# Optimization experiments

Measured on AMD Instinct MI355X. Metric: run time of the kernel, lower is better.

The kernel has to match this reference:

```python
import jax, jax.numpy as jnp
import numpy as np

B, N, C, NT = 32, 512, 32, 24   # batch, frames, channels-per-token, tokens
H, DH = 8, 48                   # heads, dim_head (DH % NT == 0 -> CS = 2)
E = H * DH                      # encode_dim = 384
IN = C * NT                     # in_dim = 768
OUT = 768                       # out_dim


def setup_inputs() -> dict:
    key = jax.random.key(0)
    ks = jax.random.split(key, 12)
    s = lambda fan_in: 1.0 / np.sqrt(fan_in)
    return {
        "x": jax.random.normal(ks[0], (B, N, C, NT), dtype=jnp.float32),
        "Wqkv_t": jax.random.uniform(ks[1], (IN, 3 * E), jnp.float32, -s(IN), s(IN)),
        "bqkv_t": jax.random.uniform(ks[2], (3 * E,), jnp.float32, -s(IN), s(IN)),
        "Wqkv_s": jax.random.uniform(ks[3], (IN, 3 * E), jnp.float32, -s(IN), s(IN)),
        "bqkv_s": jax.random.uniform(ks[4], (3 * E,), jnp.float32, -s(IN), s(IN)),
        "Wts": jax.random.uniform(ks[5], (2 * E, 2 * E), jnp.float32, -s(2 * E), s(2 * E)),
        "bts": jax.random.uniform(ks[6], (2 * E,), jnp.float32, -s(2 * E), s(2 * E)),
        "Wfc_t": jax.random.uniform(ks[7], (E, OUT), jnp.float32, -s(E), s(E)),
        "bfc_t": jax.random.uniform(ks[8], (OUT,), jnp.float32, -s(E), s(E)),
        "Wfc_s": jax.random.uniform(ks[9], (E, OUT), jnp.float32, -s(E), s(E)),
        "bfc_s": jax.random.uniform(ks[10], (OUT,), jnp.float32, -s(E), s(E)),
    }


def reference(x, Wqkv_t, bqkv_t, Wqkv_s, bqkv_s, Wts, bts, Wfc_t, bfc_t, Wfc_s, bfc_s):
    b, n, c, nt = x.shape
    cs = DH // nt  # channels per token inside a head (=2)
    xf = x.reshape(b, n, c * nt)                       # (b, n, in_dim)

    # --- temporal attention over the n (frame) axis ---
    qkv_t = (xf @ Wqkv_t + bqkv_t).reshape(b, n, 3, H, DH)
    qkv_t = jnp.transpose(qkv_t, (2, 0, 3, 1, 4))      # (3, b, H, n, DH)
    qt, kt, vt = qkv_t[0], qkv_t[1], qkv_t[2]
    attn_t = jax.nn.softmax(
        jnp.einsum('bhnd,bhmd->bhnm', qt, kt) / jnp.sqrt(jnp.float32(DH)), axis=-1)
    x_t = jnp.einsum('bhnm,bhmd->bnhd', attn_t, vt).reshape(b, n, E)

    # --- spatial attention over the nt (token) axis (note: unscaled, per source) ---
    qkv_s = (xf @ Wqkv_s + bqkv_s).reshape(b, n, 3, H, DH)
    qkv_s = jnp.transpose(qkv_s, (2, 0, 1, 3, 4)).reshape(3, b * n, H, cs, nt)
    qs, ks_, vs = qkv_s[0], qkv_s[1], qkv_s[2]         # (b*n, H, cs, nt)
    attn_s = jax.nn.softmax(jnp.einsum('ghct,ghcu->ghtu', qs, ks_), axis=-1)
    x_s = jnp.einsum('ghtu,ghcu->ghct', attn_s, vs)     # (b*n, H, cs, nt)
    x_s = x_s.reshape(b * n, H, cs * nt).reshape(b, n, E)

    # --- learned gating fusion ---
    alpha = jnp.concatenate([x_t, x_s], axis=-1).mean(axis=1, keepdims=True)  # (b,1,2E)
    alpha = (alpha @ Wts + bts).reshape(b, 1, E, 2)
    alpha = jax.nn.softmax(alpha, axis=-1)
    y = (x_t * alpha[:, :, :, 0]) @ Wfc_t + bfc_t + (x_s * alpha[:, :, :, 1]) @ Wfc_s + bfc_s
    return y  # dropout is identity in inference
```

## Files before the change

### kernel.cpp

```cpp
#include <hip/hip_runtime.h>
#include <hip/hip_bf16.h>


typedef __attribute__((ext_vector_type(8))) short s16x8;
typedef __attribute__((ext_vector_type(4))) float f32x4;

__device__ __forceinline__ float lo2f(uint u) { return __uint_as_float(u << 16); }
__device__ __forceinline__ float hi2f(uint u) { return __uint_as_float(u & 0xffff0000u); }
__device__ __forceinline__ ushort f2bu(float f) {
    union { __hip_bfloat16 h; ushort u; } c; c.h = __float2bfloat16(f); return c.u;
}
__device__ __forceinline__ uint pk2(float a, float b) {
    return (uint)f2bu(a) | ((uint)f2bu(b) << 16);
}
__device__ __forceinline__ void gload16(const void* g, void* l) {
    __builtin_amdgcn_global_load_lds((const __attribute__((address_space(1))) void*)g,
                                     (__attribute__((address_space(3))) void*)l, 16, 0, 0);
}

__device__ __forceinline__ void transpose_blk(
    const float* __restrict__ W, ushort* __restrict__ Bt,
    int task, int KT, int N, int Kt, int koff, int noff, float (*t)[33])
{
    const int k0 = (task % KT) * 32;
    const int n0 = (task / KT) * 32;
    const int r = threadIdx.x >> 3, cq = threadIdx.x & 7;
    float4 v = *(const float4*)(W + (size_t)(k0 + r) * N + n0 + cq * 4);
    t[r][cq * 4 + 0] = v.x; t[r][cq * 4 + 1] = v.y;
    t[r][cq * 4 + 2] = v.z; t[r][cq * 4 + 3] = v.w;
    __syncthreads();
    ushort4 o;
    o.x = f2bu(t[cq * 4 + 0][r]); o.y = f2bu(t[cq * 4 + 1][r]);
    o.z = f2bu(t[cq * 4 + 2][r]); o.w = f2bu(t[cq * 4 + 3][r]);
    *(ushort4*)(Bt + (size_t)(noff + n0 + r) * Kt + koff + k0 + cq * 4) = o;
}

__global__ __launch_bounds__(256) void prep(
    const float* __restrict__ x, ushort* __restrict__ xb,
    const float* __restrict__ bqkv_t, const float* __restrict__ bqkv_s,
    float* __restrict__ bias2,
    const float* __restrict__ Wqkv_t, const float* __restrict__ Wqkv_s,
    ushort* __restrict__ wbuf,
    const float* __restrict__ Wfc_t, const float* __restrict__ Wfc_s,
    ushort* __restrict__ wbuf2)
{
    __shared__ float t[32][33];
    const int bid = blockIdx.x;
    if (bid < 6144) {
        const int i = bid * 256 + threadIdx.x;
        const float4* p = (const float4*)x + (size_t)i * 2;
        float4 a = p[0], b = p[1];
        uint4 o;
        o.x = pk2(a.x, a.y); o.y = pk2(a.z, a.w);
        o.z = pk2(b.x, b.y); o.w = pk2(b.z, b.w);
        ((uint4*)xb)[i] = o;
    } else if (bid < 6153) {
        const int i = (bid - 6144) * 256 + threadIdx.x;
        bias2[i] = (i < 1152) ? bqkv_t[i] : bqkv_s[i - 1152];
    } else if (bid < 7017) {
        transpose_blk(Wqkv_t, wbuf, bid - 6153, 24, 1152, 768, 0, 0, t);
    } else if (bid < 7881) {
        transpose_blk(Wqkv_s, wbuf, bid - 7017, 24, 1152, 768, 0, 1152, t);
    } else if (bid < 8169) {
        transpose_blk(Wfc_t, wbuf2, bid - 7881, 12, 768, 768, 0, 0, t);
    } else {
        transpose_blk(Wfc_s, wbuf2, bid - 8169, 12, 768, 768, 384, 0, t);
    }
}

template<int OUTBF16, int NBIAS>
__global__ __launch_bounds__(256, 2) void gemm128p(
    const ushort* __restrict__ A, const ushort* __restrict__ Bt,
    const float* __restrict__ bias0, const float* __restrict__ bias1,
    void* __restrict__ Cout, int M, int N, int K)
{
    __shared__ ushort smem[32768];
    const int tid = threadIdx.x;
    const int m0 = blockIdx.x * 128;
    const int n0 = blockIdx.y * 128;
    const int lane = tid & 63;
    const int wr = tid >> 7;
    const int wc = (tid >> 6) & 1;
    const int lr = lane & 15;
    const int g = lane >> 4;

    f32x4 acc[4][4];
#pragma unroll
    for (int i = 0; i < 4; ++i)
#pragma unroll
        for (int j = 0; j < 4; ++j) acc[i][j] = (f32x4){0.f, 0.f, 0.f, 0.f};

    int rowT[4], kqs[4];
#pragma unroll
    for (int i = 0; i < 4; ++i) {
        const int task = tid + 256 * i;
        rowT[i] = task >> 3;
        kqs[i] = (task & 7) ^ (rowT[i] & 7);
    }

    auto stage = [&](int buf, int k0) {
        ushort* dA = &smem[buf * 16384];
        ushort* dB = &smem[buf * 16384 + 8192];
#pragma unroll
        for (int i = 0; i < 4; ++i) {
            gload16(A + (size_t)(m0 + rowT[i]) * K + k0 + (kqs[i] << 3),
                    dA + (tid + 256 * i) * 8);
            gload16(Bt + (size_t)(n0 + rowT[i]) * K + k0 + (kqs[i] << 3),
                    dB + (tid + 256 * i) * 8);
        }
    };

    stage(0, 0);
    const int nt = K >> 6;
    for (int t = 0; t < nt; ++t) {
        const int cur = t & 1;
        if (t + 1 < nt) {
            stage(cur ^ 1, (t + 1) << 6);
            asm volatile("s_waitcnt vmcnt(8)" ::: "memory");
        } else {
            asm volatile("s_waitcnt vmcnt(0)" ::: "memory");
        }
        __builtin_amdgcn_sched_barrier(0);
        __builtin_amdgcn_s_barrier();
        __builtin_amdgcn_sched_barrier(0);

        const ushort* As = &smem[cur * 16384];
        const ushort* Bs = &smem[cur * 16384 + 8192];
#pragma unroll
        for (int half = 0; half < 2; ++half) {
            s16x8 af[4], bfv[4];
#pragma unroll
            for (int i = 0; i < 4; ++i) {
                const int row = wr * 64 + 16 * i + lr;
                af[i] = *(const s16x8*)&As[row * 64
                         + (((4 * half + g) ^ (row & 7)) << 3)];
            }
#pragma unroll
            for (int j = 0; j < 4; ++j) {
                const int row = wc * 64 + 16 * j + lr;
                bfv[j] = *(const s16x8*)&Bs[row * 64
                          + (((4 * half + g) ^ (row & 7)) << 3)];
            }
#pragma unroll
            for (int i = 0; i < 4; ++i)
#pragma unroll
                for (int j = 0; j < 4; ++j)
                    acc[i][j] = __builtin_amdgcn_mfma_f32_16x16x32_bf16(
                        af[i], bfv[j], acc[i][j], 0, 0, 0);
        }
        __builtin_amdgcn_sched_barrier(0);
        __builtin_amdgcn_s_barrier();
    }

    const int c0 = n0 + wc * 64 + lr;
    float bsum[4];
#pragma unroll
    for (int j = 0; j < 4; ++j) {
        bsum[j] = bias0[c0 + 16 * j];
        if (NBIAS == 2) bsum[j] += bias1[c0 + 16 * j];
    }
    const int r0 = m0 + wr * 64 + g * 4;
#pragma unroll
    for (int i = 0; i < 4; ++i) {
        const int row = r0 + 16 * i;
#pragma unroll
        for (int j = 0; j < 4; ++j) {
            const int col = c0 + 16 * j;
#pragma unroll
            for (int v = 0; v < 4; ++v) {
                const float val = acc[i][j][v] + bsum[j];
                if (OUTBF16)
                    ((ushort*)Cout)[(size_t)(row + v) * N + col] = f2bu(val);
                else
                    ((float*)Cout)[(size_t)(row + v) * N + col] = val;
            }
        }
    }
}

__global__ __launch_bounds__(256, 4) void attn_temporal(
    const ushort* __restrict__ qkv, ushort* __restrict__ xcat)
{
    const int wg = blockIdx.x;
    const int cx = wg & 7, rx = wg >> 3;
    const int id = ((rx >> 2) << 5) + 4 * cx + (rx & 3);
    const int qt = id & 3;
    const int h = (id >> 2) & 7;
    const int b = id >> 5;

    const int tid = threadIdx.x;
    const int w = tid >> 6;
    const int lane = tid & 63;
    const int lr = lane & 15;
    const int g = lane >> 4;

    __shared__ ushort Ks[64 * 64];
    __shared__ ushort Vt[48 * 64];
    __shared__ ushort Pl[4][32 * 72];
    uint* KsU = (uint*)Ks;
    uint* VtU = (uint*)Vt;

    ((uint4*)Ks)[tid] = make_uint4(0u, 0u, 0u, 0u);
    ((uint4*)Ks)[256 + tid] = make_uint4(0u, 0u, 0u, 0u);
    __syncthreads();

    const uint* qkvu = (const uint*)qkv;
    const int qrow0 = qt * 128 + w * 32;

    s16x8 qf[2][2];
#pragma unroll
    for (int n = 0; n < 2; ++n) {
        const size_t rb = (size_t)(b * 512 + qrow0 + 16 * n + lr) * 2304 + h * 48 + 8 * g;
        qf[n][0] = *(const s16x8*)(qkv + rb);
        qf[n][1] = (g < 2) ? *(const s16x8*)(qkv + rb + 32)
                           : (s16x8){0, 0, 0, 0, 0, 0, 0, 0};
    }

    int p_[3], du_[3];
#pragma unroll
    for (int i = 0; i < 3; ++i) {
        const int idx = tid + 256 * i;
        p_[i] = idx / 24;
        du_[i] = idx % 24;
    }
    uint rk[3][2], rv[3][2];

    auto stage_load = [&](int kv0) {
#pragma unroll
        for (int i = 0; i < 3; ++i) {
            const uint* s0 = qkvu + (size_t)(b * 512 + kv0 + 2 * p_[i]) * 1152
                                  + 192 + h * 24 + du_[i];
            rk[i][0] = s0[0];    rk[i][1] = s0[1152];
            rv[i][0] = s0[192];  rv[i][1] = s0[192 + 1152];
        }
    };
    auto stage_write = [&]() {
#pragma unroll
        for (int i = 0; i < 3; ++i) {
            const int p = p_[i], du = du_[i];
            KsU[(2 * p) * 32 + ((((du >> 2) ^ ((2 * p) & 7)) << 2) | (du & 3))] = rk[i][0];
            KsU[(2 * p + 1) * 32 + ((((du >> 2) ^ ((2 * p + 1) & 7)) << 2) | (du & 3))] = rk[i][1];
            const uint w0 = (rv[i][0] & 0xffffu) | (rv[i][1] << 16);
            const uint w1 = (rv[i][0] >> 16) | (rv[i][1] & 0xffff0000u);
            const int vb = (((p >> 2) ^ (du & 7)) << 2) | (p & 3);
            VtU[(2 * du) * 32 + vb] = w0;
            VtU[(2 * du + 1) * 32 + vb] = w1;
        }
    };

    f32x4 o[2][3];
#pragma unroll
    for (int mq = 0; mq < 2; ++mq)
#pragma unroll
        for (int nd = 0; nd < 3; ++nd) o[mq][nd] = (f32x4){0.f, 0.f, 0.f, 0.f};
    float mrun[2] = {-3.0e38f, -3.0e38f};
    float lsum[2] = {0.f, 0.f};
    float corrv[2];
    const float scale = 0.14433756729740643f;

    stage_load(0);
    stage_write();
    __syncthreads();

    for (int t = 0; t < 8; ++t) {
        if (t < 7) stage_load((t + 1) * 64);

        f32x4 sa[4][2];
#pragma unroll
        for (int m = 0; m < 4; ++m)
#pragma unroll
            for (int n = 0; n < 2; ++n) sa[m][n] = (f32x4){0.f, 0.f, 0.f, 0.f};
        __builtin_amdgcn_s_setprio(1);
#pragma unroll
        for (int ks = 0; ks < 2; ++ks)
#pragma unroll
            for (int m = 0; m < 4; ++m) {
                s16x8 kf = *(const s16x8*)&Ks[(16 * m + lr) * 64
                                              + (((g + 4 * ks) ^ (lr & 7)) << 3)];
#pragma unroll
                for (int n = 0; n < 2; ++n)
                    sa[m][n] = __builtin_amdgcn_mfma_f32_16x16x32_bf16(
                        kf, qf[n][ks], sa[m][n], 0, 0, 0);
            }
        __builtin_amdgcn_s_setprio(0);

#pragma unroll
        for (int n = 0; n < 2; ++n) {
            float tmax = -3.0e38f;
#pragma unroll
            for (int m = 0; m < 4; ++m)
#pragma unroll
                for (int v = 0; v < 4; ++v) tmax = fmaxf(tmax, sa[m][n][v]);
            tmax = fmaxf(tmax, __shfl_xor(tmax, 16));
            tmax = fmaxf(tmax, __shfl_xor(tmax, 32));
            float mnew = fmaxf(mrun[n], tmax * scale);
            float corr = __expf(mrun[n] - mnew);
            mrun[n] = mnew;
            float psum = 0.f;
#pragma unroll
            for (int m = 0; m < 4; ++m) {
                float p0 = __expf(fmaf(sa[m][n][0], scale, -mnew));
                float p1 = __expf(fmaf(sa[m][n][1], scale, -mnew));
                float p2 = __expf(fmaf(sa[m][n][2], scale, -mnew));
                float p3 = __expf(fmaf(sa[m][n][3], scale, -mnew));
                psum += (p0 + p1) + (p2 + p3);
                const int base = (16 * n + lr) * 72 + 16 * m + 4 * g;
                *(uint*)&Pl[w][base] = pk2(p0, p1);
                *(uint*)&Pl[w][base + 2] = pk2(p2, p3);
            }
            psum += __shfl_xor(psum, 16);
            psum += __shfl_xor(psum, 32);
            lsum[n] = lsum[n] * corr + psum;
            corrv[n] = corr;
        }

#pragma unroll
        for (int mq = 0; mq < 2; ++mq)
#pragma unroll
            for (int nd = 0; nd < 3; ++nd)
#pragma unroll
                for (int v = 0; v < 4; ++v) o[mq][nd][v] *= corrv[mq];

        __builtin_amdgcn_s_setprio(1);
#pragma unroll
        for (int ks = 0; ks < 2; ++ks) {
            s16x8 vf[3];
#pragma unroll
            for (int nd = 0; nd < 3; ++nd)
                vf[nd] = *(const s16x8*)&Vt[(16 * nd + lr) * 64
                                            + (((g + 4 * ks) ^ (lr >> 1)) << 3)];
#pragma unroll
            for (int mq = 0; mq < 2; ++mq) {
                s16x8 pf = *(const s16x8*)&Pl[w][(16 * mq + lr) * 72 + 8 * g + 32 * ks];
#pragma unroll
                for (int nd = 0; nd < 3; ++nd)
                    o[mq][nd] = __builtin_amdgcn_mfma_f32_16x16x32_bf16(
                        vf[nd], pf, o[mq][nd], 0, 0, 0);
            }
        }
        __builtin_amdgcn_s_setprio(0);
        __syncthreads();
        if (t < 7) stage_write();
        __syncthreads();
    }

#pragma unroll
    for (int mq = 0; mq < 2; ++mq) {
        const float li = 1.f / lsum[mq];
        const int qrow = qrow0 + 16 * mq + lr;
        ushort* dst = xcat + (size_t)(b * 512 + qrow) * 768 + h * 48;
#pragma unroll
        for (int nd = 0; nd < 3; ++nd) {
            uint2 o2;
            o2.x = pk2(o[mq][nd][0] * li, o[mq][nd][1] * li);
            o2.y = pk2(o[mq][nd][2] * li, o[mq][nd][3] * li);
            *(uint2*)(dst + 16 * nd + 4 * g) = o2;
        }
    }
}

__global__ __launch_bounds__(192) void attn_spatial(
    const ushort* __restrict__ qkv, ushort* __restrict__ xcat)
{
    const int g = blockIdx.x;
    __shared__ float row[1152];
    const uint* qkvu = (const uint*)qkv;
#pragma unroll
    for (int i = 0; i < 3; ++i) {
        int idx = threadIdx.x + 192 * i;
        uint u = qkvu[(size_t)g * 1152 + 576 + idx];
        row[2 * idx] = lo2f(u); row[2 * idx + 1] = hi2f(u);
    }
    __syncthreads();

    const int h = threadIdx.x / 24;
    const int t = threadIdx.x % 24;
    const float* q = &row[h * 48];
    const float* k = &row[384 + h * 48];
    const float* v = &row[768 + h * 48];
    const float q0 = q[t], q1 = q[24 + t];

    float s[24];
    float mx = -3.0e38f;
#pragma unroll
    for (int u = 0; u < 24; ++u) {
        s[u] = q0 * k[u] + q1 * k[24 + u];
        mx = fmaxf(mx, s[u]);
    }
    float l = 0.f;
#pragma unroll
    for (int u = 0; u < 24; ++u) { s[u] = __expf(s[u] - mx); l += s[u]; }
    const float inv = 1.f / l;
    float o0 = 0.f, o1 = 0.f;
#pragma unroll
    for (int u = 0; u < 24; ++u) {
        o0 = fmaf(s[u], v[u], o0);
        o1 = fmaf(s[u], v[24 + u], o1);
    }
    ushort* dst = xcat + (size_t)g * 768 + 384 + h * 48;
    dst[t] = f2bu(o0 * inv);
    dst[24 + t] = f2bu(o1 * inv);
}

__global__ __launch_bounds__(256) void colsum(
    const ushort* __restrict__ xcat, float* __restrict__ partial)
{
    const int b = blockIdx.x, ch = blockIdx.y, part = blockIdx.z;
    const int e = ch * 256 + threadIdx.x;
    const int n0 = part * 64;
    float s = 0.f;
    for (int n = 0; n < 64; ++n)
        s += __uint_as_float((uint)xcat[((size_t)(b * 512 + n0 + n)) * 768 + e] << 16);
    partial[((size_t)(b * 8 + part)) * 768 + e] = s;
}

__global__ __launch_bounds__(256) void alpha_gate(
    const float* __restrict__ partial, const float* __restrict__ Wts,
    const float* __restrict__ bts, float* __restrict__ gate)
{
    const int b = blockIdx.x;
    const int j0 = blockIdx.y * 128;
    __shared__ float av[768];
    __shared__ float psum[2][128];

    for (int i = threadIdx.x; i < 768; i += 256) {
        float s = 0.f;
#pragma unroll
        for (int p = 0; p < 8; ++p)
            s += partial[((size_t)(b * 8 + p)) * 768 + i];
        av[i] = s * (1.0f / 512.0f);
    }
    __syncthreads();

    const int jl = threadIdx.x & 127;
    const int seg = threadIdx.x >> 7;
    const int j = j0 + jl;
    const float* Wp = Wts + (size_t)(seg * 384) * 768 + j;
    const float* avp = av + seg * 384;
    float a0 = 0.f, a1 = 0.f, a2 = 0.f, a3 = 0.f;
    float a4 = 0.f, a5 = 0.f, a6 = 0.f, a7 = 0.f;
#pragma unroll 4
    for (int k = 0; k < 384; k += 8) {
        a0 = fmaf(avp[k + 0], Wp[(size_t)(k + 0) * 768], a0);
        a1 = fmaf(avp[k + 1], Wp[(size_t)(k + 1) * 768], a1);
        a2 = fmaf(avp[k + 2], Wp[(size_t)(k + 2) * 768], a2);
        a3 = fmaf(avp[k + 3], Wp[(size_t)(k + 3) * 768], a3);
        a4 = fmaf(avp[k + 4], Wp[(size_t)(k + 4) * 768], a4);
        a5 = fmaf(avp[k + 5], Wp[(size_t)(k + 5) * 768], a5);
        a6 = fmaf(avp[k + 6], Wp[(size_t)(k + 6) * 768], a6);
        a7 = fmaf(avp[k + 7], Wp[(size_t)(k + 7) * 768], a7);
    }
    psum[seg][jl] = ((a0 + a1) + (a2 + a3)) + ((a4 + a5) + (a6 + a7));
    __syncthreads();

    if (threadIdx.x < 128)
        av[threadIdx.x] = psum[0][threadIdx.x] + psum[1][threadIdx.x]
                        + bts[j0 + threadIdx.x];
    __syncthreads();
    if (threadIdx.x < 64) {
        const int e = (j0 >> 1) + threadIdx.x;
        float x0 = av[2 * threadIdx.x], x1 = av[2 * threadIdx.x + 1];
        float m = fmaxf(x0, x1);
        float e0 = __expf(x0 - m), e1 = __expf(x1 - m);
        float inv = 1.f / (e0 + e1);
        gate[(size_t)b * 768 + e] = e0 * inv;
        gate[(size_t)b * 768 + 384 + e] = e1 * inv;
    }
}

__global__ __launch_bounds__(256) void gate_mul(
    const ushort* __restrict__ xcat, const float* __restrict__ gate,
    ushort* __restrict__ xg)
{
    const int i = blockIdx.x * 256 + threadIdx.x;
    const int m = i / 96;
    const int k = (i % 96) * 8;
    const int b = m >> 9;
    uint4 u = ((const uint4*)xcat)[i];
    const float* g = gate + (size_t)b * 768 + k;
    float4 g0 = *(const float4*)g;
    float4 g1 = *(const float4*)(g + 4);
    uint4 o;
    o.x = pk2(lo2f(u.x) * g0.x, hi2f(u.x) * g0.y);
    o.y = pk2(lo2f(u.y) * g0.z, hi2f(u.y) * g0.w);
    o.z = pk2(lo2f(u.z) * g1.x, hi2f(u.z) * g1.y);
    o.w = pk2(lo2f(u.w) * g1.z, hi2f(u.w) * g1.w);
    ((uint4*)xg)[i] = o;
}

extern "C" void kernel_launch(void* const* d_in, const int* in_sizes, int n_in,
                              void* d_out, int out_size, void* d_ws, size_t ws_size,
                              hipStream_t stream)
{
    const float* x      = (const float*)d_in[0];
    const float* Wqkv_t = (const float*)d_in[1];
    const float* bqkv_t = (const float*)d_in[2];
    const float* Wqkv_s = (const float*)d_in[3];
    const float* bqkv_s = (const float*)d_in[4];
    const float* Wts    = (const float*)d_in[5];
    const float* bts    = (const float*)d_in[6];
    const float* Wfc_t  = (const float*)d_in[7];
    const float* bfc_t  = (const float*)d_in[8];
    const float* Wfc_s  = (const float*)d_in[9];
    const float* bfc_s  = (const float*)d_in[10];
    float* out = (float*)d_out;

    char* w = (char*)d_ws;
    ushort* qkv2   = (ushort*)(w);
    ushort* xg     = qkv2;
    ushort* xcat   = (ushort*)(w + 75497472);
    ushort* xb     = (ushort*)(w + 100663296);
    ushort* wbuf   = (ushort*)(w + 125829120);
    ushort* wbuf2  = (ushort*)(w + 129368064);
    float*  partial= (float*)(w + 130547712);
    float*  gate   = (float*)(w + 131334144);
    float*  bias2  = (float*)(w + 131432448);

    const dim3 blk256(256);

    prep<<<dim3(8457), blk256, 0, stream>>>(
        x, xb, bqkv_t, bqkv_s, bias2, Wqkv_t, Wqkv_s, wbuf, Wfc_t, Wfc_s, wbuf2);

    gemm128p<1, 1><<<dim3(128, 18), blk256, 0, stream>>>(
        xb, wbuf, bias2, nullptr, qkv2, 16384, 2304, 768);

    attn_temporal<<<dim3(1024), blk256, 0, stream>>>(qkv2, xcat);
    attn_spatial<<<dim3(16384), dim3(192), 0, stream>>>(qkv2, xcat);

    colsum<<<dim3(32, 3, 8), blk256, 0, stream>>>(xcat, partial);
    alpha_gate<<<dim3(32, 6), blk256, 0, stream>>>(partial, Wts, bts, gate);
    gate_mul<<<dim3(6144), blk256, 0, stream>>>(xcat, gate, xg);

    gemm128p<0, 2><<<dim3(128, 6), blk256, 0, stream>>>(
        xg, wbuf2, bfc_t, bfc_s, out, 16384, 768, 768);
}
```

Before: 190.4 us.

## Merge spatial attention into temporal attention launch and skip small rescales

```diff
diff --git a/kernel.cpp b/kernel.cpp
--- a/kernel.cpp
+++ b/kernel.cpp
@@ -178,9 +178,58 @@
     }
 }
 
-__global__ __launch_bounds__(256, 4) void attn_temporal(
+__global__ __launch_bounds__(256, 4) void attn_fused(
     const ushort* __restrict__ qkv, ushort* __restrict__ xcat)
 {
+    __shared__ ushort Ks[64 * 64];
+    __shared__ ushort Vt[48 * 64];
+    __shared__ ushort Pl[4][32 * 72];
+    const int tid = threadIdx.x;
+    const uint* qkvu = (const uint*)qkv;
+
+    if (blockIdx.x >= 1024) {
+        const int g = blockIdx.x - 1024;
+        float* row = (float*)Ks;
+        if (tid < 192) {
+#pragma unroll
+            for (int i = 0; i < 3; ++i) {
+                int idx = tid + 192 * i;
+                uint u = qkvu[(size_t)g * 1152 + 576 + idx];
+                row[2 * idx] = lo2f(u); row[2 * idx + 1] = hi2f(u);
+            }
+        }
+        __syncthreads();
+        if (tid < 192) {
+            const int h = tid / 24;
+            const int t = tid % 24;
+            const float* q = &row[h * 48];
+            const float* k = &row[384 + h * 48];
+            const float* v = &row[768 + h * 48];
+            const float q0 = q[t], q1 = q[24 + t];
+            float s[24];
+            float mx = -3.0e38f;
+#pragma unroll
+            for (int u = 0; u < 24; ++u) {
+                s[u] = q0 * k[u] + q1 * k[24 + u];
+                mx = fmaxf(mx, s[u]);
+            }
+            float l = 0.f;
+#pragma unroll
+            for (int u = 0; u < 24; ++u) { s[u] = __expf(s[u] - mx); l += s[u]; }
+            const float inv = 1.f / l;
+            float o0 = 0.f, o1 = 0.f;
+#pragma unroll
+            for (int u = 0; u < 24; ++u) {
+                o0 = fmaf(s[u], v[u], o0);
+                o1 = fmaf(s[u], v[24 + u], o1);
+            }
+            ushort* dst = xcat + (size_t)g * 768 + 384 + h * 48;
+            dst[t] = f2bu(o0 * inv);
+            dst[24 + t] = f2bu(o1 * inv);
+        }
+        return;
+    }
+
     const int wg = blockIdx.x;
     const int cx = wg & 7, rx = wg >> 3;
     const int id = ((rx >> 2) << 5) + 4 * cx + (rx & 3);
@@ -188,15 +237,10 @@
     const int h = (id >> 2) & 7;
     const int b = id >> 5;
 
-    const int tid = threadIdx.x;
     const int w = tid >> 6;
     const int lane = tid & 63;
     const int lr = lane & 15;
     const int g = lane >> 4;
-
-    __shared__ ushort Ks[64 * 64];
-    __shared__ ushort Vt[48 * 64];
-    __shared__ ushort Pl[4][32 * 72];
     uint* KsU = (uint*)Ks;
     uint* VtU = (uint*)Vt;
 
@@ -204,7 +248,6 @@
     ((uint4*)Ks)[256 + tid] = make_uint4(0u, 0u, 0u, 0u);
     __syncthreads();
 
-    const uint* qkvu = (const uint*)qkv;
     const int qrow0 = qt * 128 + w * 32;
 
     s16x8 qf[2][2];
@@ -284,6 +327,7 @@
             }
         __builtin_amdgcn_s_setprio(0);
 
+        bool nogrow[2];
 #pragma unroll
         for (int n = 0; n < 2; ++n) {
             float tmax = -3.0e38f;
@@ -293,8 +337,10 @@
                 for (int v = 0; v < 4; ++v) tmax = fmaxf(tmax, sa[m][n][v]);
             tmax = fmaxf(tmax, __shfl_xor(tmax, 16));
             tmax = fmaxf(tmax, __shfl_xor(tmax, 32));
-            float mnew = fmaxf(mrun[n], tmax * scale);
-            float corr = __expf(mrun[n] - mnew);
+            const float tmax_s = tmax * scale;
+            nogrow[n] = __all(tmax_s <= mrun[n] + 4.f);
+            float mnew = nogrow[n] ? mrun[n] : fmaxf(mrun[n], tmax_s);
+            float corr = nogrow[n] ? 1.f : __expf(mrun[n] - mnew);
             mrun[n] = mnew;
             float psum = 0.f;
 #pragma unroll
@@ -314,12 +360,14 @@
             corrv[n] = corr;
         }
 
-#pragma unroll
-        for (int mq = 0; mq < 2; ++mq)
-#pragma unroll
-            for (int nd = 0; nd < 3; ++nd)
-#pragma unroll
-                for (int v = 0; v < 4; ++v) o[mq][nd][v] *= corrv[mq];
+        if (!(nogrow[0] && nogrow[1])) {
+#pragma unroll
+            for (int mq = 0; mq < 2; ++mq)
+#pragma unroll
+                for (int nd = 0; nd < 3; ++nd)
+#pragma unroll
+                    for (int v = 0; v < 4; ++v) o[mq][nd][v] *= corrv[mq];
+        }
 
         __builtin_amdgcn_s_setprio(1);
 #pragma unroll
@@ -357,49 +405,6 @@
             *(uint2*)(dst + 16 * nd + 4 * g) = o2;
         }
     }
-}
-
-__global__ __launch_bounds__(192) void attn_spatial(
-    const ushort* __restrict__ qkv, ushort* __restrict__ xcat)
-{
-    const int g = blockIdx.x;
-    __shared__ float row[1152];
-    const uint* qkvu = (const uint*)qkv;
-#pragma unroll
-    for (int i = 0; i < 3; ++i) {
-        int idx = threadIdx.x + 192 * i;
-        uint u = qkvu[(size_t)g * 1152 + 576 + idx];
-        row[2 * idx] = lo2f(u); row[2 * idx + 1] = hi2f(u);
-    }
-    __syncthreads();
-
-    const int h = threadIdx.x / 24;
-    const int t = threadIdx.x % 24;
-    const float* q = &row[h * 48];
-    const float* k = &row[384 + h * 48];
-    const float* v = &row[768 + h * 48];
-    const float q0 = q[t], q1 = q[24 + t];
-
-    float s[24];
-    float mx = -3.0e38f;
-#pragma unroll
-    for (int u = 0; u < 24; ++u) {
-        s[u] = q0 * k[u] + q1 * k[24 + u];
-        mx = fmaxf(mx, s[u]);
-    }
-    float l = 0.f;
-#pragma unroll
-    for (int u = 0; u < 24; ++u) { s[u] = __expf(s[u] - mx); l += s[u]; }
-    const float inv = 1.f / l;
-    float o0 = 0.f, o1 = 0.f;
-#pragma unroll
-    for (int u = 0; u < 24; ++u) {
-        o0 = fmaf(s[u], v[u], o0);
-        o1 = fmaf(s[u], v[24 + u], o1);
-    }
-    ushort* dst = xcat + (size_t)g * 768 + 384 + h * 48;
-    dst[t] = f2bu(o0 * inv);
-    dst[24 + t] = f2bu(o1 * inv);
 }
 
 __global__ __launch_bounds__(256) void colsum(
@@ -524,8 +529,7 @@
     gemm128p<1, 1><<<dim3(128, 18), blk256, 0, stream>>>(
         xb, wbuf, bias2, nullptr, qkv2, 16384, 2304, 768);
 
-    attn_temporal<<<dim3(1024), blk256, 0, stream>>>(qkv2, xcat);
-    attn_spatial<<<dim3(16384), dim3(192), 0, stream>>>(qkv2, xcat);
+    attn_fused<<<dim3(17408), blk256, 0, stream>>>(qkv2, xcat);
 
     colsum<<<dim3(32, 3, 8), blk256, 0, stream>>>(xcat, partial);
     alpha_gate<<<dim3(32, 6), blk256, 0, stream>>>(partial, Wts, bts, gate);
```

New measurement: 190.2 us. About the same (-0.1%).
